# Kernel tuning notes

Measured on AMD Instinct MI355X. Metric: run time of the kernel, lower is better.

The kernel has to match this reference:

```python
import jax, jax.numpy as jnp
import numpy as np

N_NODES = 100_000
N_EDGES = 1_600_000
D_IN, D_HID = 128, 256


def setup_inputs() -> dict:
    key = jax.random.key(0)
    k1, k2, k3, k4, k5 = jax.random.split(key, 5)
    x = jax.random.normal(k1, (N_NODES, D_IN), dtype=jnp.float32)
    edge_index = jax.random.randint(k2, (2, N_EDGES), 0, N_NODES, dtype=jnp.int64)
    # PyG Linear weights are [out_features, in_features]; glorot-ish scale
    W1 = jax.random.normal(k3, (D_HID, D_IN), dtype=jnp.float32) * (1.0 / np.sqrt(D_IN))
    W2 = jax.random.normal(k4, (D_HID, D_HID), dtype=jnp.float32) * (1.0 / np.sqrt(D_HID))
    W3 = jax.random.normal(k5, (D_HID, D_HID), dtype=jnp.float32) * (1.0 / np.sqrt(D_HID))
    return {"x": x, "edge_index": edge_index, "W1": W1, "W2": W2, "W3": W3}


def reference(x, edge_index, W1, W2, W3):
    N = x.shape[0]
    loop = jnp.arange(N, dtype=edge_index.dtype)
    # GCNConv default: add self-loops, symmetric normalization D^-1/2 (A+I) D^-1/2
    row = jnp.concatenate([edge_index[0], loop])  # source nodes
    col = jnp.concatenate([edge_index[1], loop])  # target nodes (aggregation)
    deg = jax.ops.segment_sum(jnp.ones(row.shape[0], dtype=x.dtype), col, num_segments=N)
    dinv = jnp.where(deg > 0, deg ** -0.5, 0.0)
    norm = dinv[row] * dinv[col]  # [E+N]

    def gcn_conv(h, W):
        h = h @ W.T                              # dense transform [N, out]
        msg = h[row] * norm[:, None]             # gather + scale   [E+N, out]
        return jax.ops.segment_sum(msg, col, num_segments=N)  # scatter-add

    h = jax.nn.relu(gcn_conv(x, W1))
    h = jax.nn.relu(gcn_conv(h, W2))
    return gcn_conv(h, W3)
```

## Files before the change

### kernel.cpp

```cpp
#include <hip/hip_runtime.h>


constexpr int DIN = 128;
constexpr int DH  = 256;

typedef _Float16 f16x8 __attribute__((ext_vector_type(8)));
typedef float    f32x4 __attribute__((ext_vector_type(4)));
typedef unsigned short us4 __attribute__((ext_vector_type(4)));

__device__ __forceinline__ float h2f(unsigned short u) {
    _Float16 h;
    __builtin_memcpy(&h, &u, 2);
    return (float)h;
}
__device__ __forceinline__ unsigned short f2h(float f) {
    _Float16 h = (_Float16)f;
    unsigned short u;
    __builtin_memcpy(&u, &h, 2);
    return u;
}

__global__ void zero_int_kernel(int* __restrict__ p, int n) {
    int i = blockIdx.x * blockDim.x + threadIdx.x;
    if (i < n) p[i] = 0;
}

__global__ void count_deg_kernel(const int* __restrict__ col, int E,
                                 int* __restrict__ deg, int* __restrict__ seq) {
    int i = blockIdx.x * blockDim.x + threadIdx.x;
    int base = i * 4;
    if (base >= E) return;
    if (base + 4 <= E && (((size_t)col & 15) == 0)) {
        int4 c = *(const int4*)(col + base);
        int4 s;
        s.x = atomicAdd(&deg[c.x], 1);
        s.y = atomicAdd(&deg[c.y], 1);
        s.z = atomicAdd(&deg[c.z], 1);
        s.w = atomicAdd(&deg[c.w], 1);
        *(int4*)(seq + base) = s;
    } else {
        for (int e = base; e < E && e < base + 4; ++e)
            seq[e] = atomicAdd(&deg[col[e]], 1);
    }
}

__global__ __launch_bounds__(256) void scan_p1_kernel(const int* __restrict__ deg,
                                                      int* __restrict__ bsum, int N) {
    int t = threadIdx.x;
    int base = blockIdx.x * 1024 + t * 4;
    int s = 0;
    #pragma unroll
    for (int k = 0; k < 4; k++) { int i = base + k; if (i < N) s += deg[i]; }
    __shared__ int red[256];
    red[t] = s;
    __syncthreads();
    for (int off = 128; off > 0; off >>= 1) {
        if (t < off) red[t] += red[t + off];
        __syncthreads();
    }
    if (t == 0) bsum[blockIdx.x] = red[0];
}

__global__ __launch_bounds__(1024) void scan_p2_kernel(int* __restrict__ bsum, int nb) {
    __shared__ int sums[1024];
    int t = threadIdx.x;
    int chunk = (nb + 1023) / 1024;
    int s0 = t * chunk, s1 = min(nb, s0 + chunk);
    int local = 0;
    for (int i = s0; i < s1; i++) local += bsum[i];
    sums[t] = local;
    __syncthreads();
    for (int off = 1; off < 1024; off <<= 1) {
        int v = (t >= off) ? sums[t - off] : 0;
        __syncthreads();
        sums[t] += v;
        __syncthreads();
    }
    int prefix = (t == 0) ? 0 : sums[t - 1];
    for (int i = s0; i < s1; i++) { int v = bsum[i]; bsum[i] = prefix; prefix += v; }
}

__global__ __launch_bounds__(256) void scan_p3_kernel(const int* __restrict__ deg,
                                                      const int* __restrict__ bsum,
                                                      int* __restrict__ rowptr,
                                                      float* __restrict__ dinv,
                                                      int N, int E) {
    int t = threadIdx.x;
    int base = blockIdx.x * 1024 + t * 4;
    int v[4];
    int s = 0;
    #pragma unroll
    for (int k = 0; k < 4; k++) {
        int i = base + k;
        v[k] = (i < N) ? deg[i] : 0;
        s += v[k];
    }
    __shared__ int sums[256];
    sums[t] = s;
    __syncthreads();
    for (int off = 1; off < 256; off <<= 1) {
        int u = (t >= off) ? sums[t - off] : 0;
        __syncthreads();
        sums[t] += u;
        __syncthreads();
    }
    int prefix = bsum[blockIdx.x] + ((t == 0) ? 0 : sums[t - 1]);
    #pragma unroll
    for (int k = 0; k < 4; k++) {
        int i = base + k;
        if (i < N) {
            rowptr[i] = prefix;
            dinv[i] = 1.0f / sqrtf((float)(v[k] + 1));
        }
        prefix += v[k];
    }
    if (blockIdx.x == 0 && t == 0) rowptr[N] = E;
}

__global__ void fill_csr_kernel(const int* __restrict__ row, const int* __restrict__ col,
                                const int* __restrict__ seq, const int* __restrict__ rowptr,
                                int* __restrict__ csr_src, int E) {
    int i = blockIdx.x * blockDim.x + threadIdx.x;
    int base = i * 4;
    if (base >= E) return;
    if (base + 4 <= E && (((size_t)col & 15) == 0)) {
        int4 c = *(const int4*)(col + base);
        int4 s = *(const int4*)(seq + base);
        int4 r = *(const int4*)(row + base);
        csr_src[rowptr[c.x] + s.x] = r.x;
        csr_src[rowptr[c.y] + s.y] = r.y;
        csr_src[rowptr[c.z] + s.z] = r.z;
        csr_src[rowptr[c.w] + s.w] = r.w;
    } else {
        for (int e = base; e < E && e < base + 4; ++e)
            csr_src[rowptr[col[e]] + seq[e]] = row[e];
    }
}

__global__ void cast_f16_scaled_kernel(const float4* __restrict__ in,
                                       const float* __restrict__ dinv,
                                       ushort4* __restrict__ out, int n4) {
    int i = blockIdx.x * blockDim.x + threadIdx.x;
    if (i >= n4) return;
    float s = dinv[i >> 5];
    float4 v = in[i];
    ushort4 o;
    o.x = f2h(v.x * s); o.y = f2h(v.y * s); o.z = f2h(v.z * s); o.w = f2h(v.w * s);
    out[i] = o;
}

__global__ void cast_weights_kernel(const float4* __restrict__ W1,
                                    const float4* __restrict__ W2,
                                    const float4* __restrict__ W3,
                                    ushort4* __restrict__ w1h,
                                    ushort4* __restrict__ w2h,
                                    ushort4* __restrict__ w3h) {
    int i = blockIdx.x * blockDim.x + threadIdx.x;
    const float4* src; ushort4* dst; int j = i;
    if (j < 8192)       { src = W1; dst = w1h; }
    else if (j < 24576) { src = W2; dst = w2h; j -= 8192; }
    else if (j < 40960) { src = W3; dst = w3h; j -= 24576; }
    else return;
    float4 v = src[j];
    ushort4 o;
    o.x = f2h(v.x); o.y = f2h(v.y); o.z = f2h(v.z); o.w = f2h(v.w);
    dst[j] = o;
}

template<int D>
__global__ __launch_bounds__(256) void agg_gather_f16_kernel(const int* __restrict__ rowptr,
                                                             const int* __restrict__ csr_src,
                                                             const float* __restrict__ dinv,
                                                             const us4* __restrict__ in,
                                                             us4* __restrict__ out, int N) {
    constexpr int L = D / 4;
    constexpr int GPB = 256 / L;
    int n = blockIdx.x * GPB + threadIdx.x / L;
    if (n >= N) return;
    int lane = threadIdx.x % L;

    us4 sv = __builtin_nontemporal_load(&in[(size_t)n * L + lane]);
    float4 acc = make_float4(h2f(sv.x), h2f(sv.y), h2f(sv.z), h2f(sv.w));

    int start = rowptr[n], end = rowptr[n + 1];
    for (int j0 = start; j0 < end; j0 += L) {
        int nb = end - j0; if (nb > L) nb = L;
        int src = (lane < nb) ? csr_src[j0 + lane] : 0;

        int t = 0;
        for (; t + 8 <= nb; t += 8) {
            int rr[8];
            #pragma unroll
            for (int u = 0; u < 8; ++u) {
                if constexpr (L == 64) rr[u] = __builtin_amdgcn_readlane(src, t + u);
                else                   rr[u] = __shfl(src, t + u, L);
            }
            us4 vv[8];
            #pragma unroll
            for (int u = 0; u < 8; ++u)
                vv[u] = __builtin_nontemporal_load(&in[(size_t)rr[u] * L + lane]);
            #pragma unroll
            for (int u = 0; u < 8; ++u) {
                acc.x += h2f(vv[u].x);
                acc.y += h2f(vv[u].y);
                acc.z += h2f(vv[u].z);
                acc.w += h2f(vv[u].w);
            }
        }
        for (; t < nb; ++t) {
            int r;
            if constexpr (L == 64) r = __builtin_amdgcn_readlane(src, t);
            else                   r = __shfl(src, t, L);
            us4 v = __builtin_nontemporal_load(&in[(size_t)r * L + lane]);
            acc.x += h2f(v.x); acc.y += h2f(v.y);
            acc.z += h2f(v.z); acc.w += h2f(v.w);
        }
    }
    float s = dinv[n];
    us4 o;
    o.x = f2h(acc.x * s); o.y = f2h(acc.y * s); o.z = f2h(acc.z * s); o.w = f2h(acc.w * s);
    out[(size_t)n * L + lane] = o;
}

template<int K, bool RELU, bool SCALE, typename OT>
__global__ __launch_bounds__(256) void gemm_nt_mfma_kernel(const unsigned short* __restrict__ A,
                                                           const unsigned short* __restrict__ Wh,
                                                           OT* __restrict__ C,
                                                           const float* __restrict__ dinv, int N) {
    __shared__ __align__(16) unsigned short As[128 * 64];
    __shared__ __align__(16) unsigned short Ws[128 * 64];
    int tid  = threadIdx.x;
    int lane = tid & 63;
    int wave = tid >> 6;
    int wr = wave >> 1, wc = wave & 1;

    int nwgx = (N + 127) / 128;
    int T = (2 * nwgx) & ~15;
    int b = blockIdx.x;
    int cx, cy;
    if (b < T) { cx = (b >> 4) * 8 + (b & 7); cy = (b >> 3) & 1; }
    else       { int rem = b - T; cx = (T >> 1) + (rem >> 1); cy = rem & 1; }
    int m0 = cx * 128;
    int c0 = cy * 128;

    f32x4 acc[4][4];
    #pragma unroll
    for (int i = 0; i < 4; i++)
        #pragma unroll
        for (int j = 0; j < 4; j++)
            #pragma unroll
            for (int r = 0; r < 4; r++) acc[i][j][r] = 0.0f;

    int srow  = tid >> 3;
    int sslot = tid & 7;

    for (int k0 = 0; k0 < K; k0 += 64) {
        #pragma unroll
        for (int q = 0; q < 4; ++q) {
            int row = q * 32 + srow;
            int byteoff = row * 128 + ((sslot ^ (row & 7)) << 4);
            int gr = m0 + row;
            if (gr >= N) gr = N - 1;
            f16x8 va = *(const f16x8*)(A + (size_t)gr * K + k0 + sslot * 8);
            *(f16x8*)((char*)As + byteoff) = va;
            int gw = c0 + row;
            f16x8 vw = *(const f16x8*)(Wh + (size_t)gw * K + k0 + sslot * 8);
            *(f16x8*)((char*)Ws + byteoff) = vw;
        }
        __syncthreads();

        #pragma unroll
        for (int kk = 0; kk < 2; ++kk) {
            int slot = kk * 4 + (lane >> 4);
            f16x8 a[4], bfr[4];
            #pragma unroll
            for (int i = 0; i < 4; i++) {
                int row = wr * 64 + i * 16 + (lane & 15);
                a[i] = *(const f16x8*)((const char*)As + row * 128 + ((slot ^ (row & 7)) << 4));
            }
            #pragma unroll
            for (int j = 0; j < 4; j++) {
                int row = wc * 64 + j * 16 + (lane & 15);
                bfr[j] = *(const f16x8*)((const char*)Ws + row * 128 + ((slot ^ (row & 7)) << 4));
            }
            #pragma unroll
            for (int i = 0; i < 4; i++)
                #pragma unroll
                for (int j = 0; j < 4; j++)
                    acc[i][j] = __builtin_amdgcn_mfma_f32_16x16x32_f16(a[i], bfr[j], acc[i][j], 0, 0, 0);
        }
        __syncthreads();
    }

    int r4 = (lane >> 4) * 4;
    int cn = lane & 15;
    #pragma unroll
    for (int i = 0; i < 4; i++) {
        #pragma unroll
        for (int r = 0; r < 4; r++) {
            int g_r = m0 + wr * 64 + i * 16 + r4 + r;
            if (g_r >= N) continue;
            float dv = SCALE ? dinv[g_r] : 1.0f;
            #pragma unroll
            for (int j = 0; j < 4; j++) {
                float v = acc[i][j][r];
                if (RELU) v = fmaxf(v, 0.f);
                if (SCALE) v *= dv;
                int col = c0 + wc * 64 + j * 16 + cn;
                if constexpr (sizeof(OT) == 4) {
                    ((float*)C)[(size_t)g_r * DH + col] = v;
                } else {
                    ((unsigned short*)C)[(size_t)g_r * DH + col] = f2h(v);
                }
            }
        }
    }
}

extern "C" void kernel_launch(void* const* d_in, const int* in_sizes, int n_in,
                              void* d_out, int out_size, void* d_ws, size_t ws_size,
                              hipStream_t stream) {
    const float* x  = (const float*)d_in[0];
    const int*   ei = (const int*)d_in[1];
    const float* W1 = (const float*)d_in[2];
    const float* W2 = (const float*)d_in[3];
    const float* W3 = (const float*)d_in[4];
    float* out = (float*)d_out;

    int N = in_sizes[0] / DIN;
    int E = in_sizes[1] / 2;
    const int* row = ei;
    const int* col = ei + E;

    char* ws = (char*)d_ws;
    int*   deg     = (int*)ws;
    float* dinv    = (float*)(ws + 400000);
    int*   rowptr  = (int*)(ws + 800000);
    int*   csr_src = (int*)(ws + 1200016);
    int*   seq     = (int*)(ws + 7600016);
    unsigned short* bufA = (unsigned short*)(ws + 14000128);
    unsigned short* w1h  = (unsigned short*)(ws + 65200128);
    unsigned short* w2h  = (unsigned short*)(ws + 65265664);
    unsigned short* w3h  = (unsigned short*)(ws + 65396736);
    int*   bsum    = (int*)(ws + 65527808);

    unsigned short* hb = (unsigned short*)d_out;

    dim3 b256(256);
    int nb = (N + 1023) / 1024;

    zero_int_kernel<<<dim3((N + 255) / 256), b256, 0, stream>>>(deg, N);
    count_deg_kernel<<<dim3(((E + 3) / 4 + 255) / 256), b256, 0, stream>>>(col, E, deg, seq);
    scan_p1_kernel<<<dim3(nb), b256, 0, stream>>>(deg, bsum, N);
    scan_p2_kernel<<<dim3(1), dim3(1024), 0, stream>>>(bsum, nb);
    scan_p3_kernel<<<dim3(nb), b256, 0, stream>>>(deg, bsum, rowptr, dinv, N, E);
    fill_csr_kernel<<<dim3(((E + 3) / 4 + 255) / 256), b256, 0, stream>>>(
        row, col, seq, rowptr, csr_src, E);

    cast_f16_scaled_kernel<<<dim3((N * (DIN / 4) + 255) / 256), b256, 0, stream>>>(
        (const float4*)x, dinv, (ushort4*)hb, N * (DIN / 4));
    cast_weights_kernel<<<dim3(160), b256, 0, stream>>>(
        (const float4*)W1, (const float4*)W2, (const float4*)W3,
        (ushort4*)w1h, (ushort4*)w2h, (ushort4*)w3h);

    int nwg = 2 * ((N + 127) / 128);

    agg_gather_f16_kernel<DIN><<<dim3((N + 7) / 8), b256, 0, stream>>>(
        rowptr, csr_src, dinv, (const us4*)hb, (us4*)bufA, N);
    gemm_nt_mfma_kernel<DIN, true, true, unsigned short><<<dim3(nwg), b256, 0, stream>>>(
        bufA, w1h, hb, dinv, N);

    agg_gather_f16_kernel<DH><<<dim3((N + 3) / 4), b256, 0, stream>>>(
        rowptr, csr_src, dinv, (const us4*)hb, (us4*)bufA, N);
    gemm_nt_mfma_kernel<DH, true, true, unsigned short><<<dim3(nwg), b256, 0, stream>>>(
        bufA, w2h, hb, dinv, N);

    agg_gather_f16_kernel<DH><<<dim3((N + 3) / 4), b256, 0, stream>>>(
        rowptr, csr_src, dinv, (const us4*)hb, (us4*)bufA, N);
    gemm_nt_mfma_kernel<DH, false, false, float><<<dim3(nwg), b256, 0, stream>>>(
        bufA, w3h, out, dinv, N);
}
```

Measured before the change: 750.5 us.

## Split aggregation feature columns across paired blocks and drop nontemporal loads

The gather-aggregate kernel now assigns each node's feature row to two blocks, each handling half the columns, so twice as many nodes are in flight per block and neighbor gathers touch half-row segments. Nontemporal loads are replaced with normal cached loads so repeatedly gathered rows can hit in cache. The change doubles index reads (rowptr/csr_src per half) and issues more, smaller gather requests per edge.

```diff
diff --git a/kernel.cpp b/kernel.cpp
--- a/kernel.cpp
+++ b/kernel.cpp
@@ -173,13 +173,16 @@
                                                              const float* __restrict__ dinv,
                                                              const us4* __restrict__ in,
                                                              us4* __restrict__ out, int N) {
-    constexpr int L = D / 4;
+    constexpr int L = D / 8;
     constexpr int GPB = 256 / L;
-    int n = blockIdx.x * GPB + threadIdx.x / L;
+    int b = blockIdx.x;
+    int half = b & 1;
+    int n = (b >> 1) * GPB + threadIdx.x / L;
     if (n >= N) return;
     int lane = threadIdx.x % L;
-
-    us4 sv = __builtin_nontemporal_load(&in[(size_t)n * L + lane]);
+    int off = half * L + lane;
+
+    us4 sv = in[(size_t)n * (2 * L) + off];
     float4 acc = make_float4(h2f(sv.x), h2f(sv.y), h2f(sv.z), h2f(sv.w));
 
     int start = rowptr[n], end = rowptr[n + 1];
@@ -191,14 +194,10 @@
         for (; t + 8 <= nb; t += 8) {
             int rr[8];
             #pragma unroll
-            for (int u = 0; u < 8; ++u) {
-                if constexpr (L == 64) rr[u] = __builtin_amdgcn_readlane(src, t + u);
-                else                   rr[u] = __shfl(src, t + u, L);
-            }
+            for (int u = 0; u < 8; ++u) rr[u] = __shfl(src, t + u, L);
             us4 vv[8];
             #pragma unroll
-            for (int u = 0; u < 8; ++u)
-                vv[u] = __builtin_nontemporal_load(&in[(size_t)rr[u] * L + lane]);
+            for (int u = 0; u < 8; ++u) vv[u] = in[(size_t)rr[u] * (2 * L) + off];
             #pragma unroll
             for (int u = 0; u < 8; ++u) {
                 acc.x += h2f(vv[u].x);
@@ -208,10 +207,8 @@
             }
         }
         for (; t < nb; ++t) {
-            int r;
-            if constexpr (L == 64) r = __builtin_amdgcn_readlane(src, t);
-            else                   r = __shfl(src, t, L);
-            us4 v = __builtin_nontemporal_load(&in[(size_t)r * L + lane]);
+            int r = __shfl(src, t, L);
+            us4 v = in[(size_t)r * (2 * L) + off];
             acc.x += h2f(v.x); acc.y += h2f(v.y);
             acc.z += h2f(v.z); acc.w += h2f(v.w);
         }
@@ -219,7 +216,7 @@
     float s = dinv[n];
     us4 o;
     o.x = f2h(acc.x * s); o.y = f2h(acc.y * s); o.z = f2h(acc.z * s); o.w = f2h(acc.w * s);
-    out[(size_t)n * L + lane] = o;
+    out[(size_t)n * (2 * L) + off] = o;
 }
 
 template<int K, bool RELU, bool SCALE, typename OT>
@@ -365,17 +362,20 @@
 
     int nwg = 2 * ((N + 127) / 128);
 
-    agg_gather_f16_kernel<DIN><<<dim3((N + 7) / 8), b256, 0, stream>>>(
+    int g128 = 2 * ((N + 15) / 16);
+    int g256 = 2 * ((N + 7) / 8);
+
+    agg_gather_f16_kernel<DIN><<<dim3(g128), b256, 0, stream>>>(
         rowptr, csr_src, dinv, (const us4*)hb, (us4*)bufA, N);
     gemm_nt_mfma_kernel<DIN, true, true, unsigned short><<<dim3(nwg), b256, 0, stream>>>(
         bufA, w1h, hb, dinv, N);
 
-    agg_gather_f16_kernel<DH><<<dim3((N + 3) / 4), b256, 0, stream>>>(
+    agg_gather_f16_kernel<DH><<<dim3(g256), b256, 0, stream>>>(
         rowptr, csr_src, dinv, (const us4*)hb, (us4*)bufA, N);
     gemm_nt_mfma_kernel<DH, true, true, unsigned short><<<dim3(nwg), b256, 0, stream>>>(
         bufA, w2h, hb, dinv, N);
 
-    agg_gather_f16_kernel<DH><<<dim3((N + 3) / 4), b256, 0, stream>>>(
+    agg_gather_f16_kernel<DH><<<dim3(g256), b256, 0, stream>>>(
         rowptr, csr_src, dinv, (const us4*)hb, (us4*)bufA, N);
     gemm_nt_mfma_kernel<DH, false, false, float><<<dim3(nwg), b256, 0, stream>>>(
         bufA, w3h, out, dinv, N);
```

After: 633.7 us. -15.6%, faster.
